# Kernel tuning notes

Measured on AMD Instinct MI355X. Metric: run time of the kernel, lower is better.

The kernel has to match this reference:

```python
import jax, jax.numpy as jnp
import numpy as np
import math

B, N, D, H = 2, 64, 256, 8
DK = D // H


def setup_inputs() -> dict:
    key = jax.random.key(0)
    ks = jax.random.split(key, 12)
    s = 1.0 / math.sqrt(D)
    inp = {
        "state": jax.random.normal(ks[0], (B, N, N, D), dtype=jnp.float32),
        "mask": jnp.zeros((B, N, N, N), dtype=bool),
        "W_lk": jax.random.normal(ks[1], (D, D), dtype=jnp.float32) * s,
        "b_lk": jnp.zeros((D,), dtype=jnp.float32),
        "W_rk": jax.random.normal(ks[2], (D, D), dtype=jnp.float32) * s,
        "b_rk": jnp.zeros((D,), dtype=jnp.float32),
        "W_lv": jax.random.normal(ks[3], (D, D), dtype=jnp.float32) * s,
        "b_lv": jnp.zeros((D,), dtype=jnp.float32),
        "W_rv": jax.random.normal(ks[4], (D, D), dtype=jnp.float32) * s,
        "b_rv": jnp.zeros((D,), dtype=jnp.float32),
        "W_o": jax.random.normal(ks[5], (D, D), dtype=jnp.float32) * s,
        "b_o": jnp.zeros((D,), dtype=jnp.float32),
    }
    return inp


def _proj(x, W, b):
    # torch nn.Linear: x @ W.T + b, then view to heads
    y = jnp.einsum('bxyd,ed->bxye', x, W) + b
    return y.reshape(B, N, N, H, DK)


def reference(state, mask, W_lk, b_lk, W_rk, b_rk, W_lv, b_lv, W_rv, b_rv, W_o, b_o):
    left_k = _proj(state, W_lk, b_lk)   # [B,N,N,H,DK]
    right_k = _proj(state, W_rk, b_rk)
    left_v = _proj(state, W_lv, b_lv)
    right_v = _proj(state, W_rv, b_rv)

    # triangle-style scores over node triples (x, a, y): [B,N,N,N,H]
    scores = jnp.einsum('bxahd,bayhd->bxayh', left_k, right_k) / math.sqrt(DK)
    scores = jnp.where(mask[..., None], jnp.float32(-1000.0), scores)
    att = jax.nn.softmax(scores, axis=2)  # softmax over intermediate node a

    # val[b,x,a,y,h,d] = left_v[b,x,a,h,d] * right_v[b,a,y,h,d] (materialized as in torch)
    val = jnp.einsum('bxahd,bayhd->bxayhd', left_v, right_v)
    x = jnp.einsum('bxayh,bxayhd->bxyhd', att, val)  # sum over a
    x = x.reshape(B, N, N, D)
    return jnp.einsum('bxyd,ed->bxye', x, W_o) + b_o
```

## Files before the change

kernel.cpp:

```cpp
#include <hip/hip_runtime.h>

#define B 2
#define N 64
#define D 256
#define H 8
#define DK 32
#define M (B * N * N)

typedef __attribute__((ext_vector_type(8))) short bf16x8;
typedef __attribute__((ext_vector_type(4))) float f32x4;
typedef __attribute__((ext_vector_type(2))) float f32x2;

#define PROJ_ELEMS (2097152)

__device__ __forceinline__ ushort f2b(float f) {
    union { float f; unsigned u; } v; v.f = f;
    unsigned r = v.u + 0x7fffu + ((v.u >> 16) & 1u);
    return (ushort)(r >> 16);
}
__device__ __forceinline__ float b2f(ushort u) {
    union { unsigned u; float f; } v; v.u = ((unsigned)u) << 16; return v.f;
}
__device__ __forceinline__ f32x2 up2(unsigned u) {
    union { unsigned u; float f; } lo, hi;
    lo.u = u << 16; hi.u = u & 0xffff0000u;
    f32x2 r; r.x = lo.f; r.y = hi.f; return r;
}

__device__ __forceinline__ void glds16(const ushort* g, ushort* l) {
    __builtin_amdgcn_global_load_lds(
        (const __attribute__((address_space(1))) unsigned int*)g,
        (__attribute__((address_space(3))) unsigned int*)l, 16, 0, 0);
}

__global__ __launch_bounds__(256) void cast_all(const float* __restrict__ state,
                                                const float* __restrict__ W_lk, const float* __restrict__ W_rk,
                                                const float* __restrict__ W_lv, const float* __restrict__ W_rv,
                                                const float* __restrict__ W_o,
                                                const float* __restrict__ b_lk, const float* __restrict__ b_rk,
                                                const float* __restrict__ b_lv, const float* __restrict__ b_rv,
                                                const float* __restrict__ b_o,
                                                ushort* __restrict__ state_bf,
                                                ushort* __restrict__ Wcat,
                                                float* __restrict__ bias_cat) {
    const int gid = blockIdx.x * 256 + threadIdx.x;
    const float* Ws[5] = {W_lk, W_rk, W_lv, W_rv, W_o};
    const float* bs[5] = {b_lk, b_rk, b_lv, b_rv, b_o};

    if (gid < 1280) bias_cat[gid] = bs[gid >> 8][gid & 255];

    if (gid < 524288) {
        float4 v = *(const float4*)&state[(size_t)gid * 4];
        ushort4 o = {f2b(v.x), f2b(v.y), f2b(v.z), f2b(v.w)};
        *(ushort4*)&state_bf[(size_t)gid * 4] = o;
    } else {
        int u = gid - 524288;
        int row = u >> 6;
        int k4 = (u & 63) * 4;
        const float* W = Ws[row >> 8];
        float4 v = *(const float4*)&W[(size_t)(row & 255) * 256 + k4];
        ushort4 o = {f2b(v.x), f2b(v.y), f2b(v.z), f2b(v.w)};
        *(ushort4*)&Wcat[(size_t)row * 256 + k4] = o;
    }
}

template <int BF16OUT, int RELAYOUT, int BM>
__global__ __launch_bounds__(256) void gemm_mfma(const ushort* __restrict__ A,
                                                 const ushort* __restrict__ Bw,
                                                 const float* __restrict__ bias,
                                                 void* __restrict__ Cv, int ldc) {
    constexpr int IR = BM / 32;
    __shared__ __align__(16) ushort As[2][2][BM * 32];
    __shared__ __align__(16) ushort Bs[2][2][128 * 32];
    const int tid = threadIdx.x;
    const int lane = tid & 63;
    const int wave = tid >> 6;
    const int wm = (wave & 1) * (BM / 2);
    const int wn = (wave >> 1) * 64;
    const int row0 = blockIdx.x * BM;
    const int col0 = blockIdx.y * 128;

    const int lr = lane >> 2;
    const int lkq = (lane & 3) * 8;

    const int arow = (BM == 128) ? (wave * 32) : (wave * 16);
    const ushort* gA0 = A + (size_t)(row0 + arow + lr) * 256 + lkq;
    const ushort* gA1 = gA0 + 16 * 256;
    const ushort* gB0 = Bw + (size_t)(col0 + wave * 32 + lr) * 256 + lkq;
    const ushort* gB1 = gB0 + 16 * 256;

    const int fr = lane & 15;
    const int fk = (lane >> 4) * 8;

    f32x4 acc[IR][4] = {};

    auto stage2 = [&](int grp) {
        const int buf = grp & 1;
#pragma unroll
        for (int p = 0; p < 2; ++p) {
            const int ko = (grp * 2 + p) * 32;
            glds16(gA0 + ko, &As[buf][p][arow * 32]);
            if (BM == 128) glds16(gA1 + ko, &As[buf][p][(arow + 16) * 32]);
            glds16(gB0 + ko, &Bs[buf][p][(wave * 32) * 32]);
            glds16(gB1 + ko, &Bs[buf][p][(wave * 32 + 16) * 32]);
        }
    };

    stage2(0);
    __syncthreads();

    for (int it = 0; it < 4; ++it) {
        if (it < 3) stage2(it + 1);
        const int buf = it & 1;
#pragma unroll
        for (int p = 0; p < 2; ++p) {
            bf16x8 af[IR], bf[4];
#pragma unroll
            for (int i = 0; i < IR; ++i)
                af[i] = *(const bf16x8*)&As[buf][p][(wm + i * 16 + fr) * 32 + fk];
#pragma unroll
            for (int j = 0; j < 4; ++j)
                bf[j] = *(const bf16x8*)&Bs[buf][p][(wn + j * 16 + fr) * 32 + fk];
#pragma unroll
            for (int i = 0; i < IR; ++i)
#pragma unroll
                for (int j = 0; j < 4; ++j)
                    acc[i][j] = __builtin_amdgcn_mfma_f32_16x16x32_bf16(af[i], bf[j], acc[i][j], 0, 0, 0);
        }
        __syncthreads();
    }

#pragma unroll
    for (int j = 0; j < 4; ++j) {
        const int col = col0 + wn + j * 16 + (lane & 15);
        const float bv = bias[col];
#pragma unroll
        for (int i = 0; i < IR; ++i) {
            const int rbase = row0 + wm + i * 16 + (lane >> 4) * 4;
#pragma unroll
            for (int r = 0; r < 4; ++r) {
                float o = acc[i][j][r] + bv;
                if (RELAYOUT) {
                    const int row = rbase + r;
                    const int bb = row >> 12, rr = row & 4095;
                    const int proj = col >> 8, hh = (col >> 5) & 7, dk = col & 31;
                    ((ushort*)Cv)[(size_t)proj * PROJ_ELEMS +
                                  ((size_t)(bb * 8 + hh) * 4096 + rr) * 32 + dk] = f2b(o);
                } else if (BF16OUT) {
                    ((ushort*)Cv)[(size_t)(rbase + r) * ldc + col] = f2b(o);
                } else {
                    ((float*)Cv)[(size_t)(rbase + r) * ldc + col] = o;
                }
            }
        }
    }
}

__global__ __launch_bounds__(512, 2) void fused_attn(const ushort* __restrict__ P,
                                                     const unsigned char* __restrict__ mask,
                                                     ushort* __restrict__ xbuf) {
    __shared__ __align__(16) ushort LKb[2][16 * 512];
    __shared__ __align__(16) ushort RKb[2][16 * 512];
    __shared__ __align__(16) ushort LVb[2][16 * 512];
    __shared__ __align__(16) ushort RVb[2][16 * 512];
    __shared__ __align__(16) float atts[16 * 16 * 20];
    __shared__ float mstate[16 * 20];
    __shared__ float alphas[16 * 20];

    const int bh = blockIdx.z;
    const int b = bh >> 3, h = bh & 7;
    const int x0 = blockIdx.x * 16, y0 = blockIdx.y * 16;
    const int tid = threadIdx.x;
    const int lane = tid & 63, wave = tid >> 6;

    const size_t HB = (size_t)bh * 4096 * 32;
    const ushort* PLK = P + HB;
    const ushort* PRK = P + (size_t)1 * PROJ_ELEMS + HB;
    const ushort* PLV = P + (size_t)2 * PROJ_ELEMS + HB;
    const ushort* PRV = P + (size_t)3 * PROJ_ELEMS + HB;

    const int gy = lane >> 2;
    const int du = lane & 3;
    const int fr = lane & 15, fk = (lane >> 4) * 8;
    const int yq = lane & 15, xq = (lane >> 4) * 4;
    const int sx = tid >> 4, sy = tid & 15;
    if (tid < 256) mstate[sx * 20 + sy] = -3.0e38f;

    const int sa = lane >> 2, soct = lane & 3;
    const int r2 = wave * 2;

    f32x2 acc[2][4] = {};
    float lacc[2] = {0.0f, 0.0f};
    const float scale = 0.17677669529663687f;

    unsigned char mreg[2][4];

#define STAGE(ac_, buf_)                                                                      \
    do {                                                                                      \
        glds16(PLK + ((size_t)(x0 + r2) * 64 + (ac_) + sa) * 32 + soct * 8,                   \
               &LKb[buf_][r2 * 512]);                                                         \
        glds16(PLK + ((size_t)(x0 + r2 + 1) * 64 + (ac_) + sa) * 32 + soct * 8,               \
               &LKb[buf_][(r2 + 1) * 512]);                                                   \
        glds16(PLV + ((size_t)(x0 + r2) * 64 + (ac_) + sa) * 32 + soct * 8,                   \
               &LVb[buf_][r2 * 512]);                                                         \
        glds16(PLV + ((size_t)(x0 + r2 + 1) * 64 + (ac_) + sa) * 32 + soct * 8,               \
               &LVb[buf_][(r2 + 1) * 512]);                                                   \
        glds16(PRK + ((size_t)((ac_) + r2) * 64 + y0 + sa) * 32 + soct * 8,                   \
               &RKb[buf_][r2 * 512]);                                                         \
        glds16(PRK + ((size_t)((ac_) + r2 + 1) * 64 + y0 + sa) * 32 + soct * 8,               \
               &RKb[buf_][(r2 + 1) * 512]);                                                   \
        glds16(PRV + ((size_t)((ac_) + r2) * 64 + y0 + sa) * 32 + soct * 8,                   \
               &RVb[buf_][r2 * 512]);                                                         \
        glds16(PRV + ((size_t)((ac_) + r2 + 1) * 64 + y0 + sa) * 32 + soct * 8,               \
               &RVb[buf_][(r2 + 1) * 512]);                                                   \
    } while (0)

#define MLOAD(ac_)                                                                            \
    do {                                                                                      \
        _Pragma("unroll") for (int aw = 0; aw < 2; ++aw)                                      \
        _Pragma("unroll") for (int rr = 0; rr < 4; ++rr)                                      \
            mreg[aw][rr] = mask[((size_t)(b * N + x0 + xq + rr) * N + (ac_) + wave * 2 + aw)  \
                                    * N + y0 + yq];                                           \
    } while (0)

    STAGE(0, 0);
    MLOAD(0);

    for (int c = 0; c < 4; ++c) {
        const int cur = c & 1;
        __syncthreads();

#pragma unroll
        for (int aw = 0; aw < 2; ++aw) {
            const int al = wave * 2 + aw;
            bf16x8 af = *(const bf16x8*)&LKb[cur][fr * 512 + al * 32 + fk];
            bf16x8 bf = *(const bf16x8*)&RKb[cur][al * 512 + fr * 32 + fk];
            f32x4 s = {};
            s = __builtin_amdgcn_mfma_f32_16x16x32_bf16(af, bf, s, 0, 0, 0);
            float4 ov;
            float* op = (float*)&ov;
#pragma unroll
            for (int rr = 0; rr < 4; ++rr) {
                float sv = s[rr] * scale;
                if (mreg[aw][rr]) sv = -1000.0f;
                op[rr] = sv;
            }
            *(float4*)&atts[(al * 16 + yq) * 20 + xq] = ov;
        }
        __syncthreads();

        if (tid < 256) {
            float mc = -3.0e38f;
#pragma unroll
            for (int a = 0; a < 16; ++a) mc = fmaxf(mc, atts[(a * 16 + sy) * 20 + sx]);
            const float mold = mstate[sx * 20 + sy];
            const float mnew = fmaxf(mold, mc);
            mstate[sx * 20 + sy] = mnew;
            alphas[sx * 20 + sy] = __expf(mold - mnew);
        }
        __syncthreads();

        if (c < 3) {
            STAGE((c + 1) * 16, cur ^ 1);
            MLOAD((c + 1) * 16);
        }

        float mn[2];
#pragma unroll
        for (int i = 0; i < 2; ++i) {
            const int x = wave * 2 + i;
            const float av = alphas[x * 20 + gy];
            mn[i] = mstate[x * 20 + gy];
            lacc[i] *= av;
#pragma unroll
            for (int q = 0; q < 4; ++q) acc[i][q] *= av;
        }

        {
            const unsigned* LV32 = (const unsigned*)&LVb[cur][0];
            const unsigned* RV32 = (const unsigned*)&RVb[cur][0];
#pragma unroll
            for (int a = 0; a < 16; ++a) {
                const uint4 lv0 = *(const uint4*)&LV32[(wave * 2) * 256 + a * 16 + du * 4];
                const uint4 lv1 = *(const uint4*)&LV32[(wave * 2 + 1) * 256 + a * 16 + du * 4];
                const uint4 rvw = *(const uint4*)&RV32[a * 256 + gy * 16 + du * 4];
                const float2 w2 = *(const float2*)&atts[(a * 16 + gy) * 20 + wave * 2];
                const float w0 = __expf(w2.x - mn[0]);
                const float w1 = __expf(w2.y - mn[1]);
                lacc[0] += w0;
                lacc[1] += w1;
                const f32x2 rv0 = up2(rvw.x), rv1 = up2(rvw.y);
                const f32x2 rv2 = up2(rvw.z), rv3 = up2(rvw.w);
                acc[0][0] += (up2(lv0.x) * w0) * rv0;
                acc[0][1] += (up2(lv0.y) * w0) * rv1;
                acc[0][2] += (up2(lv0.z) * w0) * rv2;
                acc[0][3] += (up2(lv0.w) * w0) * rv3;
                acc[1][0] += (up2(lv1.x) * w1) * rv0;
                acc[1][1] += (up2(lv1.y) * w1) * rv1;
                acc[1][2] += (up2(lv1.z) * w1) * rv2;
                acc[1][3] += (up2(lv1.w) * w1) * rv3;
            }
        }
    }

#pragma unroll
    for (int i = 0; i < 2; ++i) {
        const int x = wave * 2 + i;
        const float il = 1.0f / lacc[i];
        ushort o[8] __attribute__((aligned(16)));
#pragma unroll
        for (int q = 0; q < 4; ++q) {
            o[2 * q]     = f2b(acc[i][q].x * il);
            o[2 * q + 1] = f2b(acc[i][q].y * il);
        }
        *(uint4*)&xbuf[(((size_t)b * N + x0 + x) * N + y0 + gy) * D + h * DK + du * 8] =
            *(const uint4*)o;
    }
#undef STAGE
#undef MLOAD
}

extern "C" void kernel_launch(void* const* d_in, const int* in_sizes, int n_in,
                              void* d_out, int out_size, void* d_ws, size_t ws_size,
                              hipStream_t stream) {
    const float* state = (const float*)d_in[0];
    const unsigned char* mask = (const unsigned char*)d_in[1];
    const float* W_lk = (const float*)d_in[2];
    const float* b_lk = (const float*)d_in[3];
    const float* W_rk = (const float*)d_in[4];
    const float* b_rk = (const float*)d_in[5];
    const float* W_lv = (const float*)d_in[6];
    const float* b_lv = (const float*)d_in[7];
    const float* W_rv = (const float*)d_in[8];
    const float* b_rv = (const float*)d_in[9];
    const float* W_o = (const float*)d_in[10];
    const float* b_o = (const float*)d_in[11];
    float* out = (float*)d_out;

    char* ws = (char*)d_ws;
    ushort* P_bf = (ushort*)ws;
    ws += (size_t)4 * PROJ_ELEMS * 2;
    float* bias_cat = (float*)ws;
    ws += 1280 * 4;
    ushort* state_bf = (ushort*)ws;
    ws += (size_t)M * D * 2;
    ushort* Wcat = (ushort*)ws;
    ws += (size_t)1280 * 256 * 2;
    ushort* xbuf_bf = (ushort*)ws;

    cast_all<<<2368, 256, 0, stream>>>(state, W_lk, W_rk, W_lv, W_rv, W_o,
                                       b_lk, b_rk, b_lv, b_rv, b_o,
                                       state_bf, Wcat, bias_cat);
    gemm_mfma<1, 1, 128><<<dim3(M / 128, 8), 256, 0, stream>>>(state_bf, Wcat, bias_cat, P_bf, 1024);
    fused_attn<<<dim3(4, 4, B * H), 512, 0, stream>>>(P_bf, mask, xbuf_bf);
    gemm_mfma<0, 0, 64><<<dim3(M / 64, 2), 256, 0, stream>>>(xbuf_bf, Wcat + 1024 * 256, bias_cat + 1024, out, 256);
}
```

Before: 123.9 us.

## Double fused attention block to 1024 threads with one row per wave and padded LDS

The fused attention kernel moves from 512 to 1024 threads per block, so each wave handles one intermediate node for the score MFMA and one (x, y) output element per thread instead of two. LDS tiles for LK, LV and RV are padded to a row stride of 520, and RV is staged transposed so each thread reads its y row contiguously, aimed at cutting bank conflicts. Each staging plane is now loaded by its own group of waves. This halves per-thread registers and work to gain latency hiding, but launch bounds drop to one block per CU and there are only 256 blocks.

```diff
diff --git a/kernel.cpp b/kernel.cpp
--- a/kernel.cpp
+++ b/kernel.cpp
@@ -156,13 +156,13 @@
     }
 }
 
-__global__ __launch_bounds__(512, 2) void fused_attn(const ushort* __restrict__ P,
-                                                     const unsigned char* __restrict__ mask,
-                                                     ushort* __restrict__ xbuf) {
-    __shared__ __align__(16) ushort LKb[2][16 * 512];
+__global__ __launch_bounds__(1024, 1) void fused_attn(const ushort* __restrict__ P,
+                                                      const unsigned char* __restrict__ mask,
+                                                      ushort* __restrict__ xbuf) {
+    __shared__ __align__(16) ushort LKb[2][16 * 520];
+    __shared__ __align__(16) ushort LVb[2][16 * 520];
+    __shared__ __align__(16) ushort RVb[2][16 * 520];
     __shared__ __align__(16) ushort RKb[2][16 * 512];
-    __shared__ __align__(16) ushort LVb[2][16 * 512];
-    __shared__ __align__(16) ushort RVb[2][16 * 512];
     __shared__ __align__(16) float atts[16 * 16 * 20];
     __shared__ float mstate[16 * 20];
     __shared__ float alphas[16 * 20];
@@ -179,48 +179,47 @@
     const ushort* PLV = P + (size_t)2 * PROJ_ELEMS + HB;
     const ushort* PRV = P + (size_t)3 * PROJ_ELEMS + HB;
 
-    const int gy = lane >> 2;
-    const int du = lane & 3;
     const int fr = lane & 15, fk = (lane >> 4) * 8;
     const int yq = lane & 15, xq = (lane >> 4) * 4;
+    const int xg = wave >> 2, du = wave & 3;
+    const int xi = lane >> 4, gy = lane & 15;
+    const int gx = xg * 4 + xi;
     const int sx = tid >> 4, sy = tid & 15;
     if (tid < 256) mstate[sx * 20 + sy] = -3.0e38f;
 
+    const int splane = wave >> 2, srow0 = (wave & 3) * 4;
     const int sa = lane >> 2, soct = lane & 3;
-    const int r2 = wave * 2;
-
-    f32x2 acc[2][4] = {};
-    float lacc[2] = {0.0f, 0.0f};
+
+    f32x2 acc[4] = {};
+    float lacc = 0.0f;
     const float scale = 0.17677669529663687f;
 
-    unsigned char mreg[2][4];
+    unsigned char mreg[4];
 
 #define STAGE(ac_, buf_)                                                                      \
     do {                                                                                      \
-        glds16(PLK + ((size_t)(x0 + r2) * 64 + (ac_) + sa) * 32 + soct * 8,                   \
-               &LKb[buf_][r2 * 512]);                                                         \
-        glds16(PLK + ((size_t)(x0 + r2 + 1) * 64 + (ac_) + sa) * 32 + soct * 8,               \
-               &LKb[buf_][(r2 + 1) * 512]);                                                   \
-        glds16(PLV + ((size_t)(x0 + r2) * 64 + (ac_) + sa) * 32 + soct * 8,                   \
-               &LVb[buf_][r2 * 512]);                                                         \
-        glds16(PLV + ((size_t)(x0 + r2 + 1) * 64 + (ac_) + sa) * 32 + soct * 8,               \
-               &LVb[buf_][(r2 + 1) * 512]);                                                   \
-        glds16(PRK + ((size_t)((ac_) + r2) * 64 + y0 + sa) * 32 + soct * 8,                   \
-               &RKb[buf_][r2 * 512]);                                                         \
-        glds16(PRK + ((size_t)((ac_) + r2 + 1) * 64 + y0 + sa) * 32 + soct * 8,               \
-               &RKb[buf_][(r2 + 1) * 512]);                                                   \
-        glds16(PRV + ((size_t)((ac_) + r2) * 64 + y0 + sa) * 32 + soct * 8,                   \
-               &RVb[buf_][r2 * 512]);                                                         \
-        glds16(PRV + ((size_t)((ac_) + r2 + 1) * 64 + y0 + sa) * 32 + soct * 8,               \
-               &RVb[buf_][(r2 + 1) * 512]);                                                   \
+        _Pragma("unroll") for (int rr4 = 0; rr4 < 4; ++rr4) {                                 \
+            const int row = srow0 + rr4;                                                      \
+            if (splane == 0)                                                                  \
+                glds16(PLK + ((size_t)(x0 + row) * 64 + (ac_) + sa) * 32 + soct * 8,          \
+                       &LKb[buf_][row * 520]);                                                \
+            else if (splane == 1)                                                             \
+                glds16(PLV + ((size_t)(x0 + row) * 64 + (ac_) + sa) * 32 + soct * 8,          \
+                       &LVb[buf_][row * 520]);                                                \
+            else if (splane == 2)                                                             \
+                glds16(PRV + ((size_t)((ac_) + sa) * 64 + y0 + row) * 32 + soct * 8,          \
+                       &RVb[buf_][row * 520]);                                                \
+            else                                                                              \
+                glds16(PRK + ((size_t)((ac_) + row) * 64 + y0 + sa) * 32 + soct * 8,          \
+                       &RKb[buf_][row * 512]);                                                \
+        }                                                                                     \
     } while (0)
 
 #define MLOAD(ac_)                                                                            \
     do {                                                                                      \
-        _Pragma("unroll") for (int aw = 0; aw < 2; ++aw)                                      \
         _Pragma("unroll") for (int rr = 0; rr < 4; ++rr)                                      \
-            mreg[aw][rr] = mask[((size_t)(b * N + x0 + xq + rr) * N + (ac_) + wave * 2 + aw)  \
-                                    * N + y0 + yq];                                           \
+            mreg[rr] = mask[((size_t)(b * N + x0 + xq + rr) * N + (ac_) + wave) * N +         \
+                            y0 + yq];                                                         \
     } while (0)
 
     STAGE(0, 0);
@@ -230,11 +229,9 @@
         const int cur = c & 1;
         __syncthreads();
 
-#pragma unroll
-        for (int aw = 0; aw < 2; ++aw) {
-            const int al = wave * 2 + aw;
-            bf16x8 af = *(const bf16x8*)&LKb[cur][fr * 512 + al * 32 + fk];
-            bf16x8 bf = *(const bf16x8*)&RKb[cur][al * 512 + fr * 32 + fk];
+        {
+            bf16x8 af = *(const bf16x8*)&LKb[cur][fr * 520 + wave * 32 + fk];
+            bf16x8 bf = *(const bf16x8*)&RKb[cur][wave * 512 + fr * 32 + fk];
             f32x4 s = {};
             s = __builtin_amdgcn_mfma_f32_16x16x32_bf16(af, bf, s, 0, 0, 0);
             float4 ov;
@@ -242,10 +239,10 @@
 #pragma unroll
             for (int rr = 0; rr < 4; ++rr) {
                 float sv = s[rr] * scale;
-                if (mreg[aw][rr]) sv = -1000.0f;
+                if (mreg[rr]) sv = -1000.0f;
                 op[rr] = sv;
             }
-            *(float4*)&atts[(al * 16 + yq) * 20 + xq] = ov;
+            *(float4*)&atts[(wave * 16 + yq) * 20 + xq] = ov;
         }
         __syncthreads();
 
@@ -265,55 +262,40 @@
             MLOAD((c + 1) * 16);
         }
 
-        float mn[2];
-#pragma unroll
-        for (int i = 0; i < 2; ++i) {
-            const int x = wave * 2 + i;
-            const float av = alphas[x * 20 + gy];
-            mn[i] = mstate[x * 20 + gy];
-            lacc[i] *= av;
-#pragma unroll
-            for (int q = 0; q < 4; ++q) acc[i][q] *= av;
-        }
+        {
+            const float av = alphas[gx * 20 + gy];
+            lacc *= av;
+#pragma unroll
+            for (int q = 0; q < 4; ++q) acc[q] *= av;
+        }
+        const float mnv = mstate[gx * 20 + gy];
 
         {
             const unsigned* LV32 = (const unsigned*)&LVb[cur][0];
             const unsigned* RV32 = (const unsigned*)&RVb[cur][0];
 #pragma unroll
             for (int a = 0; a < 16; ++a) {
-                const uint4 lv0 = *(const uint4*)&LV32[(wave * 2) * 256 + a * 16 + du * 4];
-                const uint4 lv1 = *(const uint4*)&LV32[(wave * 2 + 1) * 256 + a * 16 + du * 4];
-                const uint4 rvw = *(const uint4*)&RV32[a * 256 + gy * 16 + du * 4];
-                const float2 w2 = *(const float2*)&atts[(a * 16 + gy) * 20 + wave * 2];
-                const float w0 = __expf(w2.x - mn[0]);
-                const float w1 = __expf(w2.y - mn[1]);
-                lacc[0] += w0;
-                lacc[1] += w1;
-                const f32x2 rv0 = up2(rvw.x), rv1 = up2(rvw.y);
-                const f32x2 rv2 = up2(rvw.z), rv3 = up2(rvw.w);
-                acc[0][0] += (up2(lv0.x) * w0) * rv0;
-                acc[0][1] += (up2(lv0.y) * w0) * rv1;
-                acc[0][2] += (up2(lv0.z) * w0) * rv2;
-                acc[0][3] += (up2(lv0.w) * w0) * rv3;
-                acc[1][0] += (up2(lv1.x) * w1) * rv0;
-                acc[1][1] += (up2(lv1.y) * w1) * rv1;
-                acc[1][2] += (up2(lv1.z) * w1) * rv2;
-                acc[1][3] += (up2(lv1.w) * w1) * rv3;
+                const uint4 lvw = *(const uint4*)&LV32[gx * 260 + a * 16 + du * 4];
+                const uint4 rvw = *(const uint4*)&RV32[gy * 260 + a * 16 + du * 4];
+                const float w = __expf(atts[(a * 16 + gy) * 20 + gx] - mnv);
+                lacc += w;
+                acc[0] += (up2(lvw.x) * w) * up2(rvw.x);
+                acc[1] += (up2(lvw.y) * w) * up2(rvw.y);
+                acc[2] += (up2(lvw.z) * w) * up2(rvw.z);
+                acc[3] += (up2(lvw.w) * w) * up2(rvw.w);
             }
         }
     }
 
-#pragma unroll
-    for (int i = 0; i < 2; ++i) {
-        const int x = wave * 2 + i;
-        const float il = 1.0f / lacc[i];
+    {
+        const float il = 1.0f / lacc;
         ushort o[8] __attribute__((aligned(16)));
 #pragma unroll
         for (int q = 0; q < 4; ++q) {
-            o[2 * q]     = f2b(acc[i][q].x * il);
-            o[2 * q + 1] = f2b(acc[i][q].y * il);
-        }
-        *(uint4*)&xbuf[(((size_t)b * N + x0 + x) * N + y0 + gy) * D + h * DK + du * 8] =
+            o[2 * q]     = f2b(acc[q].x * il);
+            o[2 * q + 1] = f2b(acc[q].y * il);
+        }
+        *(uint4*)&xbuf[(((size_t)b * N + x0 + gx) * N + y0 + gy) * D + h * DK + du * 8] =
             *(const uint4*)o;
     }
 #undef STAGE
@@ -352,6 +334,6 @@
                                        b_lk, b_rk, b_lv, b_rv, b_o,
                                        state_bf, Wcat, bias_cat);
     gemm_mfma<1, 1, 128><<<dim3(M / 128, 8), 256, 0, stream>>>(state_bf, Wcat, bias_cat, P_bf, 1024);
-    fused_attn<<<dim3(4, 4, B * H), 512, 0, stream>>>(P_bf, mask, xbuf_bf);
+    fused_attn<<<dim3(4, 4, B * H), 1024, 0, stream>>>(P_bf, mask, xbuf_bf);
     gemm_mfma<0, 0, 64><<<dim3(M / 64, 2), 256, 0, stream>>>(xbuf_bf, Wcat + 1024 * 256, bias_cat + 1024, out, 256);
 }
```

New measurement: 122.3 us. Within noise of the previous version (-1.3%).
